# Optimization experiments

Hardware: AMD Instinct MI355X
Metric: run time of the kernel (lower is better)

Reference implementation:

```python
import jax, jax.numpy as jnp
import numpy as np

B, C, H, W = 32, 256, 64, 64
K = 7  # kernel_size

def setup_inputs() -> dict:
    key = jax.random.key(0)
    kx, kw = jax.random.split(key)
    x = jax.random.normal(kx, (B, C, H, W), dtype=jnp.float32)
    # Conv2d(2, 1, 7, bias=False) weight: [out_ch=1, in_ch=2, 7, 7]
    w = jax.random.normal(kw, (1, 2, K, K), dtype=jnp.float32) * (1.0 / np.sqrt(2 * K * K))
    return {"x": x, "w": w}

def reference(x, w):
    # channel-wise max and mean, keepdim -> [B,1,H,W]
    max_out = jnp.max(x, axis=1, keepdims=True)
    avg_out = jnp.mean(x, axis=1, keepdims=True)
    concat = jnp.concatenate([max_out, avg_out], axis=1)  # [B,2,H,W]
    pad = K // 2
    conv = jax.lax.conv_general_dilated(
        concat, w,
        window_strides=(1, 1),
        padding=[(pad, pad), (pad, pad)],
        dimension_numbers=("NCHW", "OIHW", "NCHW"),
    )  # [B,1,H,W]
    scale = jax.nn.sigmoid(conv)
    return x * scale  # broadcast over channels
```

## Files before the change

### kernel.cpp

```cpp
#include <hip/hip_runtime.h>
#include <math.h>

constexpr int Bn  = 32;
constexpr int Cn  = 256;
constexpr int Hn  = 64;
constexpr int Wn  = 64;
constexpr int HW  = Hn * Wn;
constexpr int CHW = Cn * HW;
constexpr int HW4 = HW / 4;
constexpr int NPOS  = Bn * HW;
constexpr int NPOS4 = NPOS / 4;

constexpr int CM_ROWS  = 4;
constexpr int CM_LR    = CM_ROWS + 6;
constexpr int CM_LC    = 72;
constexpr int CM_GRID  = NPOS4 / 64;

typedef float f4_t __attribute__((ext_vector_type(4)));

__global__ __launch_bounds__(256) void reduce_k(const float* __restrict__ x,
                                                float* __restrict__ pmax,
                                                float* __restrict__ pavg) {
    __shared__ float4 smax[4][64];
    __shared__ float4 ssum[4][64];

    const int lane  = threadIdx.x & 63;
    const int chunk = threadIdx.x >> 6;
    const int pos4  = blockIdx.x * 64 + lane;
    const int b     = pos4 >> 10;
    const int sp4   = pos4 & (HW4 - 1);

    const float4* xp = (const float4*)x + (size_t)b * (CHW / 4)
                       + (size_t)(chunk * 64) * HW4 + sp4;

    float4 mx = make_float4(-INFINITY, -INFINITY, -INFINITY, -INFINITY);
    float4 sm = make_float4(0.f, 0.f, 0.f, 0.f);

    #pragma unroll 8
    for (int c = 0; c < 64; ++c) {
        float4 v = xp[(size_t)c * HW4];
        mx.x = fmaxf(mx.x, v.x); mx.y = fmaxf(mx.y, v.y);
        mx.z = fmaxf(mx.z, v.z); mx.w = fmaxf(mx.w, v.w);
        sm.x += v.x; sm.y += v.y; sm.z += v.z; sm.w += v.w;
    }

    smax[chunk][lane] = mx;
    ssum[chunk][lane] = sm;
    __syncthreads();

    if (chunk == 0) {
        float4 M = smax[0][lane];
        float4 S = ssum[0][lane];
        #pragma unroll
        for (int k = 1; k < 4; ++k) {
            float4 m2 = smax[k][lane];
            float4 s2 = ssum[k][lane];
            M.x = fmaxf(M.x, m2.x); M.y = fmaxf(M.y, m2.y);
            M.z = fmaxf(M.z, m2.z); M.w = fmaxf(M.w, m2.w);
            S.x += s2.x; S.y += s2.y; S.z += s2.z; S.w += s2.w;
        }
        const float inv = 1.0f / (float)Cn;
        float4 A = make_float4(S.x * inv, S.y * inv, S.z * inv, S.w * inv);
        ((float4*)pmax)[pos4] = M;
        ((float4*)pavg)[pos4] = A;
    }
}

__global__ __launch_bounds__(256) void convmul_k(const float* __restrict__ x,
                                                 const float* __restrict__ pmax,
                                                 const float* __restrict__ pavg,
                                                 const float* __restrict__ w,
                                                 float* __restrict__ out) {
    __shared__ float spm[CM_LR][CM_LC];
    __shared__ float spa[CM_LR][CM_LC];
    __shared__ float ssc[256];
    __shared__ float sw[98];

    const int tid = threadIdx.x;
    const int bid = blockIdx.x;
    const int b   = bid >> 4;
    const int rg  = bid & 15;
    const int row0 = rg * CM_ROWS;

    if (tid < 98) sw[tid] = w[tid];

    const float* pm = pmax + b * HW;
    const float* pa = pavg + b * HW;
    for (int i = tid; i < CM_LR * CM_LC; i += 256) {
        const int lr = i / CM_LC;
        const int lc = i % CM_LC;
        const int gh = row0 - 3 + lr;
        const int gw = lc - 3;
        const bool ok = (gh >= 0) && (gh < Hn) && (gw >= 0) && (gw < Wn);
        const float vm = ok ? pm[gh * Wn + gw] : 0.f;
        const float va = ok ? pa[gh * Wn + gw] : 0.f;
        spm[lr][lc] = vm;
        spa[lr][lc] = va;
    }
    __syncthreads();

    {
        const int hl  = tid >> 6;
        const int col = tid & 63;
        float acc = 0.f;
        #pragma unroll
        for (int kh = 0; kh < 7; ++kh) {
            #pragma unroll
            for (int kw = 0; kw < 7; ++kw) {
                acc += spm[hl + kh][col + kw] * sw[kh * 7 + kw]
                     + spa[hl + kh][col + kw] * sw[49 + kh * 7 + kw];
            }
        }
        ssc[tid] = 1.f / (1.f + expf(-acc));
    }
    __syncthreads();

    const int wv   = tid >> 6;
    const int lane = tid & 63;
    const int sp4  = rg * 64 + lane;

    const float4 s = ((const float4*)ssc)[lane];

    const float4* x4 = (const float4*)x;
    float4* o4 = (float4*)out;

    size_t idx = (size_t)b * (CHW / 4) + (size_t)(wv * 64) * HW4 + sp4;
    #pragma unroll 4
    for (int k = 0; k < 64; ++k, idx += HW4) {
        const float4 v = x4[idx];
        f4_t o;
        o.x = v.x * s.x; o.y = v.y * s.y;
        o.z = v.z * s.z; o.w = v.w * s.w;
        __builtin_nontemporal_store(o, (f4_t*)&o4[idx]);
    }
}

extern "C" void kernel_launch(void* const* d_in, const int* in_sizes, int n_in,
                              void* d_out, int out_size, void* d_ws, size_t ws_size,
                              hipStream_t stream) {
    const float* x = (const float*)d_in[0];
    const float* w = (const float*)d_in[1];
    float* out = (float*)d_out;

    float* pmax = (float*)d_ws;
    float* pavg = pmax + NPOS;

    reduce_k<<<NPOS4 / 64, 256, 0, stream>>>(x, pmax, pavg);

    convmul_k<<<CM_GRID, 256, 0, stream>>>(x, pmax, pavg, w, out);
}
```

Before: 248.5 us.

## Fuse channel reduction into conv-scale kernel with per-block halo recomputation

Merges the channel max/mean reduction kernel into the conv+sigmoid+multiply kernel. Each block now reduces all 256 channels for its 4 output rows plus a 3-row halo directly into shared memory. This removes the workspace round trip for the pooled maps and one kernel launch. In exchange, each block rereads x for 10 rows instead of 4, and only 160 threads do a long serial 256-channel loop, which lowers parallelism.

```diff
diff --git a/kernel.cpp b/kernel.cpp
--- a/kernel.cpp
+++ b/kernel.cpp
@@ -8,94 +8,58 @@
 constexpr int HW  = Hn * Wn;
 constexpr int CHW = Cn * HW;
 constexpr int HW4 = HW / 4;
-constexpr int NPOS  = Bn * HW;
-constexpr int NPOS4 = NPOS / 4;
 
-constexpr int CM_ROWS  = 4;
-constexpr int CM_LR    = CM_ROWS + 6;
-constexpr int CM_LC    = 72;
-constexpr int CM_GRID  = NPOS4 / 64;
+constexpr int RG   = 4;
+constexpr int NRG  = Hn / RG;
+constexpr int LR   = RG + 6;
+constexpr int LC   = 72;
+constexpr int GRID = Bn * NRG;
 
 typedef float f4_t __attribute__((ext_vector_type(4)));
 
-__global__ __launch_bounds__(256) void reduce_k(const float* __restrict__ x,
-                                                float* __restrict__ pmax,
-                                                float* __restrict__ pavg) {
-    __shared__ float4 smax[4][64];
-    __shared__ float4 ssum[4][64];
+__global__ __launch_bounds__(256) void fused_k(const float* __restrict__ x,
+                                               const float* __restrict__ w,
+                                               float* __restrict__ out) {
+    __shared__ float spm[LR][LC];
+    __shared__ float spa[LR][LC];
+    __shared__ float ssc[RG * Wn];
+    __shared__ float sw[98];
 
-    const int lane  = threadIdx.x & 63;
-    const int chunk = threadIdx.x >> 6;
-    const int pos4  = blockIdx.x * 64 + lane;
-    const int b     = pos4 >> 10;
-    const int sp4   = pos4 & (HW4 - 1);
+    const int tid  = threadIdx.x;
+    const int b    = blockIdx.x >> 4;
+    const int rg   = blockIdx.x & (NRG - 1);
+    const int row0 = rg * RG;
 
-    const float4* xp = (const float4*)x + (size_t)b * (CHW / 4)
-                       + (size_t)(chunk * 64) * HW4 + sp4;
-
-    float4 mx = make_float4(-INFINITY, -INFINITY, -INFINITY, -INFINITY);
-    float4 sm = make_float4(0.f, 0.f, 0.f, 0.f);
-
-    #pragma unroll 8
-    for (int c = 0; c < 64; ++c) {
-        float4 v = xp[(size_t)c * HW4];
-        mx.x = fmaxf(mx.x, v.x); mx.y = fmaxf(mx.y, v.y);
-        mx.z = fmaxf(mx.z, v.z); mx.w = fmaxf(mx.w, v.w);
-        sm.x += v.x; sm.y += v.y; sm.z += v.z; sm.w += v.w;
+    if (tid < 98) sw[tid] = w[tid];
+    for (int i = tid; i < LR * LC; i += 256) {
+        ((float*)spm)[i] = 0.f;
+        ((float*)spa)[i] = 0.f;
     }
-
-    smax[chunk][lane] = mx;
-    ssum[chunk][lane] = sm;
     __syncthreads();
 
-    if (chunk == 0) {
-        float4 M = smax[0][lane];
-        float4 S = ssum[0][lane];
-        #pragma unroll
-        for (int k = 1; k < 4; ++k) {
-            float4 m2 = smax[k][lane];
-            float4 s2 = ssum[k][lane];
-            M.x = fmaxf(M.x, m2.x); M.y = fmaxf(M.y, m2.y);
-            M.z = fmaxf(M.z, m2.z); M.w = fmaxf(M.w, m2.w);
-            S.x += s2.x; S.y += s2.y; S.z += s2.z; S.w += s2.w;
+    if (tid < LR * 16) {
+        const int lr = tid >> 4;
+        const int c4 = tid & 15;
+        const int gh = row0 - 3 + lr;
+        if (gh >= 0 && gh < Hn) {
+            const float4* xp = (const float4*)x + (size_t)b * (CHW / 4)
+                               + gh * 16 + c4;
+            float4 mx = make_float4(-INFINITY, -INFINITY, -INFINITY, -INFINITY);
+            float4 sm = make_float4(0.f, 0.f, 0.f, 0.f);
+            #pragma unroll 8
+            for (int c = 0; c < Cn; ++c) {
+                float4 v = xp[(size_t)c * HW4];
+                mx.x = fmaxf(mx.x, v.x); mx.y = fmaxf(mx.y, v.y);
+                mx.z = fmaxf(mx.z, v.z); mx.w = fmaxf(mx.w, v.w);
+                sm.x += v.x; sm.y += v.y; sm.z += v.z; sm.w += v.w;
+            }
+            const float inv = 1.0f / (float)Cn;
+            const int cb = 3 + c4 * 4;
+            spm[lr][cb + 0] = mx.x; spm[lr][cb + 1] = mx.y;
+            spm[lr][cb + 2] = mx.z; spm[lr][cb + 3] = mx.w;
+            spa[lr][cb + 0] = sm.x * inv; spa[lr][cb + 1] = sm.y * inv;
+            spa[lr][cb + 2] = sm.z * inv; spa[lr][cb + 3] = sm.w * inv;
         }
-        const float inv = 1.0f / (float)Cn;
-        float4 A = make_float4(S.x * inv, S.y * inv, S.z * inv, S.w * inv);
-        ((float4*)pmax)[pos4] = M;
-        ((float4*)pavg)[pos4] = A;
-    }
-}
-
-__global__ __launch_bounds__(256) void convmul_k(const float* __restrict__ x,
-                                                 const float* __restrict__ pmax,
-                                                 const float* __restrict__ pavg,
-                                                 const float* __restrict__ w,
-                                                 float* __restrict__ out) {
-    __shared__ float spm[CM_LR][CM_LC];
-    __shared__ float spa[CM_LR][CM_LC];
-    __shared__ float ssc[256];
-    __shared__ float sw[98];
-
-    const int tid = threadIdx.x;
-    const int bid = blockIdx.x;
-    const int b   = bid >> 4;
-    const int rg  = bid & 15;
-    const int row0 = rg * CM_ROWS;
-
-    if (tid < 98) sw[tid] = w[tid];
-
-    const float* pm = pmax + b * HW;
-    const float* pa = pavg + b * HW;
-    for (int i = tid; i < CM_LR * CM_LC; i += 256) {
-        const int lr = i / CM_LC;
-        const int lc = i % CM_LC;
-        const int gh = row0 - 3 + lr;
-        const int gw = lc - 3;
-        const bool ok = (gh >= 0) && (gh < Hn) && (gw >= 0) && (gw < Wn);
-        const float vm = ok ? pm[gh * Wn + gw] : 0.f;
-        const float va = ok ? pa[gh * Wn + gw] : 0.f;
-        spm[lr][lc] = vm;
-        spa[lr][lc] = va;
     }
     __syncthreads();
 
@@ -117,14 +81,13 @@
 
     const int wv   = tid >> 6;
     const int lane = tid & 63;
-    const int sp4  = rg * 64 + lane;
-
     const float4 s = ((const float4*)ssc)[lane];
 
     const float4* x4 = (const float4*)x;
     float4* o4 = (float4*)out;
 
-    size_t idx = (size_t)b * (CHW / 4) + (size_t)(wv * 64) * HW4 + sp4;
+    size_t idx = (size_t)b * (CHW / 4) + (size_t)(wv * 64) * HW4
+               + rg * 64 + lane;
     #pragma unroll 4
     for (int k = 0; k < 64; ++k, idx += HW4) {
         const float4 v = x4[idx];
@@ -142,10 +105,5 @@
     const float* w = (const float*)d_in[1];
     float* out = (float*)d_out;
 
-    float* pmax = (float*)d_ws;
-    float* pavg = pmax + NPOS;
-
-    reduce_k<<<NPOS4 / 64, 256, 0, stream>>>(x, pmax, pavg);
-
-    convmul_k<<<CM_GRID, 256, 0, stream>>>(x, pmax, pavg, w, out);
+    fused_k<<<GRID, 256, 0, stream>>>(x, w, out);
 }
```

Measured after the change: 267.1 us. 1.07x slower.
